# Performance work log

Measured on AMD Instinct MI355X. Metric: run time of the kernel, lower is better.

The kernel has to match this reference:

```python
import jax, jax.numpy as jnp
import numpy as np

N, R, A, F, T, O = 50000, 5, 8, 128, 2, 128
RADIUS = 1.0

def _template_vertices():
    # polar grid of template vertices in cartesian coords, shape (R, A, 2)
    radii = (np.arange(1, R + 1) / R) * RADIUS
    angles = np.linspace(0.0, 2.0 * np.pi, A, endpoint=False)
    x = radii[:, None] * np.cos(angles)[None, :]
    y = radii[:, None] * np.sin(angles)[None, :]
    return np.stack([x, y], axis=-1)

def _interp_coeffs():
    # Gaussian interpolation coefficients (concrete define_interpolation_coefficients),
    # shape (R, A, R*A), rows normalized -- constant, non-trainable (built in build()).
    v = _template_vertices().reshape(R * A, 2)
    d2 = ((v[:, None, :] - v[None, :, :]) ** 2).sum(-1)
    sigma = RADIUS / R
    w = np.exp(-d2 / (2.0 * sigma ** 2))
    w = w / w.sum(axis=1, keepdims=True)
    return w.reshape(R, A, R * A).astype(np.float32)

def setup_inputs() -> dict:
    key = jax.random.key(0)
    k1, k2, k3, k4, k5 = jax.random.split(key, 5)
    mesh_signal = jax.random.normal(k1, (N, F), dtype=jnp.float32)
    bary_w = jax.random.uniform(k2, (N, R, A, 3), dtype=jnp.float32)
    bary_w = bary_w / bary_w.sum(axis=-1, keepdims=True)  # barycentric weights sum to 1
    bary_idx = jax.random.randint(k3, (N, R, A, 3), 0, N, dtype=jnp.int32)
    glorot = lambda k, shp: jax.random.uniform(
        k, shp, jnp.float32, -1.0, 1.0) * np.sqrt(6.0 / (shp[-1] + shp[-2]))
    template_weights = glorot(k4, (A, T, O, F))  # (n_angular, templates, out, feat)
    bias = glorot(k5, (T, O))
    return {"mesh_signal": mesh_signal, "bary_w": bary_w,
            "template_weights": template_weights, "bias": bias,
            "interp_coeffs": jnp.asarray(_interp_coeffs()),
            "bary_idx": bary_idx}

def reference(mesh_signal, bary_w, template_weights, bias, interp_coeffs, bary_idx):
    # --- patch operator: barycentric gather + interpolation ---
    gathered = mesh_signal[bary_idx]                       # (N,R,A,3,F) irregular gather
    interp = (bary_w[..., None] * gathered).sum(axis=-2)   # (N,R,A,F)
    # prior: mix all R*A template-vertex signals per output template vertex
    sig = interp.reshape(-1, R * A, F)                     # (N,RA,F)
    interp = jnp.einsum('nkf,rak->nraf', sig, interp_coeffs)  # (N,R,A,F)
    # --- fold: all A rotations (rotation_delta=1), vectorized by rolling weights ---
    rots = jnp.arange(0, A, 1)                             # K = A rotations
    idx = (jnp.arange(A)[None, :] + rots[:, None]) % A     # (K,A): roll(interp,+r) == roll(W,-r)
    W_all = template_weights[idx]                          # (K,A,T,O,F)
    # TF adds bias before summing over (R,A) axes -> bias appears R*A times
    z = jnp.einsum('nraf,katof->nkto', interp, W_all) + (R * A) * bias  # (N,K,T,O)
    out = jax.nn.relu(z).sum(axis=2)                       # sum over templates -> (N,K,O)
    return out
```

## Files before the change

kernel.cpp:

```cpp
#include <hip/hip_runtime.h>
#include <hip/hip_bf16.h>
#include <stdint.h>

#define NN 50000
#define RR 5
#define AA 8
#define FF 128
#define TT 2
#define OO 128
#define KDIM 1024
#define KB 512
#define RA 40

typedef __attribute__((ext_vector_type(8))) short short8;
typedef __attribute__((ext_vector_type(4))) float f32x4;
typedef __attribute__((ext_vector_type(2))) float f32x2;
typedef __attribute__((ext_vector_type(4))) int i32x4;
typedef __attribute__((ext_vector_type(2))) unsigned u32x2;

#if __has_builtin(__builtin_elementwise_fma)
__device__ inline f32x2 pk_fma(f32x2 a, f32x2 b, f32x2 c) {
  return __builtin_elementwise_fma(a, b, c);
}
#else
__device__ inline f32x2 pk_fma(f32x2 a, f32x2 b, f32x2 c) {
  f32x2 d;
  asm("v_pk_fma_f32 %0, %1, %2, %3" : "=v"(d) : "v"(a), "v"(b), "v"(c));
  return d;
}
#endif

__device__ inline void gload_lds16(const void* g, void* l) {
  __builtin_amdgcn_global_load_lds(
      (const __attribute__((address_space(1))) unsigned int*)g,
      (__attribute__((address_space(3))) unsigned int*)l, 16, 0, 0);
}

__global__ void prep_kernel(const float* __restrict__ mesh,
                            const float* __restrict__ coeffs,
                            const float* __restrict__ W,
                            const float* __restrict__ bary_w,
                            const int* __restrict__ bary_idx,
                            __hip_bfloat16* __restrict__ meshq,
                            float* __restrict__ G,
                            __hip_bfloat16* __restrict__ B2,
                            unsigned* __restrict__ packb,
                            int do_pack) {
  int tid = blockIdx.x * blockDim.x + threadIdx.x;
  int stride = gridDim.x * blockDim.x;
  for (int i = tid; i < NN * FF; i += stride) {
    int n = i >> 7, f = i & 127;
    int p = f >> 5, fo = f & 31;
    meshq[((long)p * NN + n) * 32 + fo] = __float2bfloat16(mesh[i]);
  }
  for (int i = tid; i < AA * RA; i += stride) {
    int p = i / RA, k = i % RA;
    int a = p & 3;
    float s1 = 0.f, s2 = 0.f;
    for (int r = 0; r < RR; ++r) {
      s1 += coeffs[(r * AA + a) * RA + k];
      s2 += coeffs[(r * AA + a + 4) * RA + k];
    }
    G[i] = (p < 4) ? (s1 + s2) : (s1 - s2);
  }
  for (int e = tid; e < 2048 * KB; e += stride) {
    int sub = e & 7;
    int lane = (e >> 3) & 63;
    int kt = (e >> 9) & 15;
    int cg = (e >> 13) & 63;
    int half = e >> 19;
    int c = cg * 16 + (lane & 15);
    int k = kt * 32 + (lane >> 4) * 8 + sub;
    int o = c >> 3, t = (c >> 2) & 1, j = c & 3;
    int a4 = k >> 7, f = k & 127;
    int m = (a4 + j) & 3;
    float w0 = W[((m * TT + t) * OO + o) * FF + f];
    float w4 = W[(((m + 4) * TT + t) * OO + o) * FF + f];
    float v;
    if (half == 0) v = 0.5f * (w0 + w4);
    else {
      v = 0.5f * (w0 - w4);
      if (a4 + j >= 4) v = -v;
    }
    B2[e] = __float2bfloat16(v);
  }
  if (do_pack) {
    for (int i = tid; i < NN * 120; i += stride) {
      __hip_bfloat16 h = __float2bfloat16(bary_w[i]);
      unsigned wb = *(unsigned short*)&h;
      packb[i] = ((unsigned)bary_idx[i] << 16) | wb;
    }
  }
}

__global__ __launch_bounds__(256) void s_pass_packed(
    const __hip_bfloat16* __restrict__ meshq,
    const unsigned* __restrict__ packb,
    const float* __restrict__ G,
    __hip_bfloat16* __restrict__ Sout,
    int p) {
  __shared__ unsigned pk_s[32 * 120];
  __shared__ float g_s[AA * RA];
  int tid = threadIdx.x;
  long n0 = (long)blockIdx.x * 32;
  int nnode = (NN - n0 < 32) ? (int)(NN - n0) : 32;
  int nvec = nnode * 30;
  const i32x4* psrc = (const i32x4*)(packb + n0 * 120);
  for (int i = tid; i < nvec; i += 256) {
    i32x4 v = __builtin_nontemporal_load(psrc + i);
    ((i32x4*)pk_s)[i] = v;
  }
  for (int i = tid; i < AA * RA; i += 256) g_s[i] = G[i];
  __syncthreads();

  int g = tid >> 3;
  int fo = tid & 7;
  long n = n0 + g;
  if (n >= NN) return;
  const unsigned* pg = pk_s + g * 120;
  const char* mbase = (const char*)meshq + (long)p * NN * 64 + fo * 8;

  f32x2 accA[AA], accB[AA];
#pragma unroll
  for (int a = 0; a < AA; ++a) {
    accA[a] = (f32x2){0.f, 0.f};
    accB[a] = (f32x2){0.f, 0.f};
  }

#pragma unroll 2
  for (int k = 0; k < RA; ++k) {
    f32x2 sA = (f32x2){0.f, 0.f}, sB = (f32x2){0.f, 0.f};
#pragma unroll
    for (int j = 0; j < 3; ++j) {
      unsigned v = pg[k * 3 + j];
      long row = v >> 16;
      float w = __uint_as_float(v << 16);
      f32x2 wv = (f32x2){w, w};
      u32x2 u = *(const u32x2*)(mbase + row * 64);
      f32x2 lo = (f32x2){__uint_as_float(u[0] << 16),
                         __uint_as_float(u[0] & 0xffff0000u)};
      f32x2 hi = (f32x2){__uint_as_float(u[1] << 16),
                         __uint_as_float(u[1] & 0xffff0000u)};
      sA = pk_fma(wv, lo, sA);
      sB = pk_fma(wv, hi, sB);
    }
#pragma unroll
    for (int a = 0; a < AA; ++a) {
      float cc = g_s[a * RA + k];
      f32x2 cv = (f32x2){cc, cc};
      accA[a] = pk_fma(cv, sA, accA[a]);
      accB[a] = pk_fma(cv, sB, accB[a]);
    }
  }

  long base = n * KDIM + p * 32 + fo * 4;
#pragma unroll
  for (int a = 0; a < AA; ++a) {
    __hip_bfloat16 h0 = __float2bfloat16(accA[a][0]);
    __hip_bfloat16 h1 = __float2bfloat16(accA[a][1]);
    __hip_bfloat16 h2 = __float2bfloat16(accB[a][0]);
    __hip_bfloat16 h3 = __float2bfloat16(accB[a][1]);
    unsigned w0 = (unsigned)*(unsigned short*)&h0 |
                  ((unsigned)*(unsigned short*)&h1 << 16);
    unsigned w1 = (unsigned)*(unsigned short*)&h2 |
                  ((unsigned)*(unsigned short*)&h3 << 16);
    u32x2 st = (u32x2){w0, w1};
    __builtin_nontemporal_store(st, (u32x2*)(Sout + base + a * FF));
  }
}

__global__ __launch_bounds__(256) void s_pass_kernel(
    const __hip_bfloat16* __restrict__ meshq,
    const float* __restrict__ bary_w,
    const int* __restrict__ bary_idx,
    const float* __restrict__ G,
    __hip_bfloat16* __restrict__ Sout,
    int p) {
  __shared__ float w_s[16 * 120];
  __shared__ int i_s[16 * 120];
  __shared__ float g_s[AA * RA];
  int tid = threadIdx.x;
  long n0 = (long)blockIdx.x * 16;
  const f32x4* wsrc = (const f32x4*)(bary_w + n0 * 120);
  const i32x4* isrc = (const i32x4*)(bary_idx + n0 * 120);
  for (int i = tid; i < 480; i += 256) {
    f32x4 wv = __builtin_nontemporal_load(wsrc + i);
    ((f32x4*)w_s)[i] = wv;
    i32x4 iv = __builtin_nontemporal_load(isrc + i);
    ((i32x4*)i_s)[i] = iv;
  }
  for (int i = tid; i < AA * RA; i += 256) g_s[i] = G[i];
  __syncthreads();
  int g = tid >> 4;
  int fo = tid & 15;
  long n = n0 + g;
  const float* wg = w_s + g * 120;
  const int* ig = i_s + g * 120;
  const char* mbase = (const char*)meshq + (long)p * NN * 64 + fo * 4;
  float sx_acc[AA], sy_acc[AA];
#pragma unroll
  for (int a = 0; a < AA; ++a) { sx_acc[a] = 0.f; sy_acc[a] = 0.f; }
#pragma unroll 2
  for (int k = 0; k < RA; ++k) {
    float sx = 0.f, sy = 0.f;
#pragma unroll
    for (int j = 0; j < 3; ++j) {
      int row = ig[k * 3 + j];
      unsigned u = *(const unsigned*)(mbase + (long)row * 64);
      float w = wg[k * 3 + j];
      sx += w * __uint_as_float(u << 16);
      sy += w * __uint_as_float(u & 0xffff0000u);
    }
#pragma unroll
    for (int a = 0; a < AA; ++a) {
      float c = g_s[a * RA + k];
      sx_acc[a] += c * sx;
      sy_acc[a] += c * sy;
    }
  }
  long base = n * KDIM + p * 32 + fo * 2;
#pragma unroll
  for (int a = 0; a < AA; ++a) {
    __hip_bfloat16 hx = __float2bfloat16(sx_acc[a]);
    __hip_bfloat16 hy = __float2bfloat16(sy_acc[a]);
    unsigned u = (unsigned)*(unsigned short*)&hx | ((unsigned)*(unsigned short*)&hy << 16);
    __builtin_nontemporal_store(u, (unsigned*)(Sout + base + a * FF));
  }
}

__global__ __launch_bounds__(256, 3) void gemm_kernel(
    const __hip_bfloat16* __restrict__ Sh,
    const __hip_bfloat16* __restrict__ B2,
    const float* __restrict__ bias,
    float* __restrict__ out) {
  int bx = blockIdx.x;
  int by = blockIdx.y;
  int cb = by & 7;
  int mt = ((by >> 3) << 3) + bx;
  if (mt >= 782) return;
  int row0 = mt * 64;

  int tid = threadIdx.x;
  int lane = tid & 63;
  int wid = tid >> 6;
  int wave_m = wid >> 1;
  int wave_n = wid & 1;

  __shared__ __align__(16) char lds[49152];

  long srcA[2];
  int dstA[2];
#pragma unroll
  for (int i = 0; i < 2; ++i) {
    int li = i * 256 + tid;
    int plane = li >> 8;
    int r = (li & 255) >> 2, sp = li & 3;
    int sl = sp ^ ((r >> 1) & 3);
    int rowA = row0 + r;
    if (rowA >= NN) rowA = NN - 1;
    srcA[i] = (long)rowA * KDIM + plane * 512 + sl * 8;
    dstA[i] = li * 16;
  }
  const char* b2c = (const char*)B2;
  long srcB[4];
  int dstB[4];
#pragma unroll
  for (int i = 0; i < 4; ++i) {
    int li = i * 256 + tid;
    int half = li >> 9, cgl = (li >> 6) & 7, inner = li & 63;
    srcB[i] = (((long)(half * 64 + cb * 8 + cgl) * 16) * 1024) + inner * 16;
    dstB[i] = 8192 + li * 16;
  }
  int offA[2];
#pragma unroll
  for (int m = 0; m < 2; ++m) {
    int r = wave_m * 32 + m * 16 + (lane & 15);
    int phys = (lane >> 4) ^ ((r >> 1) & 3);
    offA[m] = r * 64 + phys * 16;
  }
  int offB[4];
#pragma unroll
  for (int n = 0; n < 4; ++n)
    offB[n] = 8192 + (wave_n * 4 + n) * 1024 + lane * 16;

  f32x4 acc[2][8];
#pragma unroll
  for (int m = 0; m < 2; ++m)
#pragma unroll
    for (int q = 0; q < 8; ++q) acc[m][q] = (f32x4){0.f, 0.f, 0.f, 0.f};

#define STAGE(T)                                                              \
  {                                                                           \
    char* base_ = lds + ((T) & 1) * 24576;                                    \
    long k0_ = (long)(T) * 32;                                                \
    _Pragma("unroll") for (int i_ = 0; i_ < 2; ++i_)                          \
        gload_lds16(Sh + srcA[i_] + k0_, base_ + dstA[i_]);                   \
    _Pragma("unroll") for (int i_ = 0; i_ < 4; ++i_)                          \
        gload_lds16(b2c + srcB[i_] + (long)(T) * 1024, base_ + dstB[i_]);     \
  }

#define GSTEP(STP, DOSTAGE)                                                   \
  {                                                                           \
    const char* cbuf = lds + ((STP) & 1) * 24576;                             \
    asm volatile("s_waitcnt vmcnt(0)" ::: "memory");                          \
    __builtin_amdgcn_sched_barrier(0);                                        \
    __builtin_amdgcn_s_barrier();                                             \
    __builtin_amdgcn_sched_barrier(0);                                        \
    if (DOSTAGE) STAGE((STP) + 1)                                             \
    __builtin_amdgcn_sched_barrier(0);                                        \
    short8 aE[2], aO[2], bE[4], bO[4];                                        \
    _Pragma("unroll") for (int m_ = 0; m_ < 2; ++m_) {                        \
      aE[m_] = *(const short8*)(cbuf + offA[m_]);                             \
      aO[m_] = *(const short8*)(cbuf + offA[m_] + 4096);                      \
    }                                                                         \
    _Pragma("unroll") for (int n_ = 0; n_ < 4; ++n_) {                        \
      bE[n_] = *(const short8*)(cbuf + offB[n_]);                             \
      bO[n_] = *(const short8*)(cbuf + offB[n_] + 8192);                      \
    }                                                                         \
    __builtin_amdgcn_s_setprio(1);                                            \
    _Pragma("unroll") for (int m_ = 0; m_ < 2; ++m_)                          \
        _Pragma("unroll") for (int n_ = 0; n_ < 4; ++n_) {                    \
      acc[m_][n_] = __builtin_amdgcn_mfma_f32_16x16x32_bf16(                  \
          aE[m_], bE[n_], acc[m_][n_], 0, 0, 0);                              \
      acc[m_][n_ + 4] = __builtin_amdgcn_mfma_f32_16x16x32_bf16(              \
          aO[m_], bO[n_], acc[m_][n_ + 4], 0, 0, 0);                          \
    }                                                                         \
    __builtin_amdgcn_s_setprio(0);                                            \
    __builtin_amdgcn_sched_barrier(0);                                        \
  }

  STAGE(0)
  GSTEP(0, 1)  GSTEP(1, 1)  GSTEP(2, 1)  GSTEP(3, 1)
  GSTEP(4, 1)  GSTEP(5, 1)  GSTEP(6, 1)  GSTEP(7, 1)
  GSTEP(8, 1)  GSTEP(9, 1)  GSTEP(10, 1) GSTEP(11, 1)
  GSTEP(12, 1) GSTEP(13, 1) GSTEP(14, 1) GSTEP(15, 0)

  __syncthreads();
  float* lout = (float*)lds;
  int c = lane & 15;
  int t = (c >> 2) & 1;
  int j = c & 3;
  int hi = lane >> 4;
  float bq[4];
#pragma unroll
  for (int n = 0; n < 4; ++n) {
    int o_l = wave_n * 8 + n * 2 + (c >> 3);
    bq[n] = 40.f * bias[t * OO + cb * 16 + o_l];
  }
#pragma unroll
  for (int m = 0; m < 2; ++m) {
#pragma unroll
    for (int n = 0; n < 4; ++n) {
      int o_l = wave_n * 8 + n * 2 + (c >> 3);
#pragma unroll
      for (int i = 0; i < 4; ++i) {
        float zE = acc[m][n][i];
        float zO = acc[m][n + 4][i];
        float rlo = fmaxf(zE + zO + bq[n], 0.f);
        float rhi = fmaxf(zE - zO + bq[n], 0.f);
        rlo += __shfl_xor(rlo, 4);
        rhi += __shfl_xor(rhi, 4);
        if (!(lane & 4)) {
          int cl = wave_m * 32 + m * 16 + hi * 4 + i;
          lout[cl * 156 + j * 20 + o_l] = rlo;
          lout[cl * 156 + (j + 4) * 20 + o_l] = rhi;
        }
      }
    }
  }
  __syncthreads();
#pragma unroll
  for (int it = 0; it < 8; ++it) {
    int gi = it * 256 + tid;
    int cl = gi >> 5;
    int rem = gi & 31;
    int kr = rem >> 2, q = rem & 3;
    int grow = row0 + cl;
    if (grow < NN) {
      f32x4 v = *(const f32x4*)(lout + cl * 156 + kr * 20 + q * 4);
      long gaddr = (long)grow * 1024 + kr * 128 + cb * 16 + q * 4;
      __builtin_nontemporal_store(v, (f32x4*)(out + gaddr));
    }
  }
}

extern "C" void kernel_launch(void* const* d_in, const int* in_sizes, int n_in,
                              void* d_out, int out_size, void* d_ws, size_t ws_size,
                              hipStream_t stream) {
  const float* mesh   = (const float*)d_in[0];
  const float* bary_w = (const float*)d_in[1];
  const float* W      = (const float*)d_in[2];
  const float* bias   = (const float*)d_in[3];
  const float* coeffs = (const float*)d_in[4];
  const int* bidx     = (const int*)d_in[5];
  float* out = (float*)d_out;
  char* ws = (char*)d_ws;

  __hip_bfloat16* meshq = (__hip_bfloat16*)ws;
  float* G              = (float*)(ws + 12800000);
  __hip_bfloat16* B2    = (__hip_bfloat16*)(ws + 12801280);
  __hip_bfloat16* Smat  = (__hip_bfloat16*)(ws + 16995584);
  unsigned* packb       = (unsigned*)(ws + 119395584);

  int do_pack = (ws_size >= 143395584UL) ? 1 : 0;

  prep_kernel<<<dim3(2048), dim3(256), 0, stream>>>(mesh, coeffs, W, bary_w, bidx,
                                                    meshq, G, B2, packb, do_pack);
  if (do_pack) {
    for (int p = 0; p < 4; ++p)
      s_pass_packed<<<dim3(1563), dim3(256), 0, stream>>>(meshq, packb, G, Smat, p);
  } else {
    for (int p = 0; p < 4; ++p)
      s_pass_kernel<<<dim3(3125), dim3(256), 0, stream>>>(meshq, bary_w, bidx, G, Smat, p);
  }
  gemm_kernel<<<dim3(8, 784), dim3(256), 0, stream>>>(Smat, B2, bias, out);
}
```

Baseline: 374.1 us.

## Split GEMM waves by K-half instead of M to reuse A fragments

Reassigns the four waves so each pair handles one half (even/odd plane) of the K data across all 64 rows, rather than splitting rows. Each wave now loads 4 A and 4 B fragments per step instead of 4 A and 8 B, which cuts LDS read traffic per MFMA. The partial accumulators of the two halves must then be combined through LDS in the epilogue, done in four row slices with extra barriers and a narrower, serialized output store phase.

```diff
diff --git a/kernel.cpp b/kernel.cpp
--- a/kernel.cpp
+++ b/kernel.cpp
@@ -243,8 +243,8 @@
   int tid = threadIdx.x;
   int lane = tid & 63;
   int wid = tid >> 6;
-  int wave_m = wid >> 1;
-  int wave_n = wid & 1;
+  int half = wid >> 1;
+  int wn = wid & 1;
 
   __shared__ __align__(16) char lds[49152];
 
@@ -267,27 +267,27 @@
 #pragma unroll
   for (int i = 0; i < 4; ++i) {
     int li = i * 256 + tid;
-    int half = li >> 9, cgl = (li >> 6) & 7, inner = li & 63;
-    srcB[i] = (((long)(half * 64 + cb * 8 + cgl) * 16) * 1024) + inner * 16;
+    int hf = li >> 9, cgl = (li >> 6) & 7, inner = li & 63;
+    srcB[i] = (((long)(hf * 64 + cb * 8 + cgl) * 16) * 1024) + inner * 16;
     dstB[i] = 8192 + li * 16;
   }
-  int offA[2];
-#pragma unroll
-  for (int m = 0; m < 2; ++m) {
-    int r = wave_m * 32 + m * 16 + (lane & 15);
+  int offA[4];
+#pragma unroll
+  for (int m = 0; m < 4; ++m) {
+    int r = m * 16 + (lane & 15);
     int phys = (lane >> 4) ^ ((r >> 1) & 3);
-    offA[m] = r * 64 + phys * 16;
+    offA[m] = half * 4096 + r * 64 + phys * 16;
   }
   int offB[4];
 #pragma unroll
   for (int n = 0; n < 4; ++n)
-    offB[n] = 8192 + (wave_n * 4 + n) * 1024 + lane * 16;
-
-  f32x4 acc[2][8];
-#pragma unroll
-  for (int m = 0; m < 2; ++m)
-#pragma unroll
-    for (int q = 0; q < 8; ++q) acc[m][q] = (f32x4){0.f, 0.f, 0.f, 0.f};
+    offB[n] = 8192 + half * 8192 + (wn * 4 + n) * 1024 + lane * 16;
+
+  f32x4 acc[4][4];
+#pragma unroll
+  for (int m = 0; m < 4; ++m)
+#pragma unroll
+    for (int n = 0; n < 4; ++n) acc[m][n] = (f32x4){0.f, 0.f, 0.f, 0.f};
 
 #define STAGE(T)                                                              \
   {                                                                           \
@@ -308,23 +308,16 @@
     __builtin_amdgcn_sched_barrier(0);                                        \
     if (DOSTAGE) STAGE((STP) + 1)                                             \
     __builtin_amdgcn_sched_barrier(0);                                        \
-    short8 aE[2], aO[2], bE[4], bO[4];                                        \
-    _Pragma("unroll") for (int m_ = 0; m_ < 2; ++m_) {                        \
-      aE[m_] = *(const short8*)(cbuf + offA[m_]);                             \
-      aO[m_] = *(const short8*)(cbuf + offA[m_] + 4096);                      \
-    }                                                                         \
-    _Pragma("unroll") for (int n_ = 0; n_ < 4; ++n_) {                        \
-      bE[n_] = *(const short8*)(cbuf + offB[n_]);                             \
-      bO[n_] = *(const short8*)(cbuf + offB[n_] + 8192);                      \
-    }                                                                         \
+    short8 aF[4], bF[4];                                                      \
+    _Pragma("unroll") for (int m_ = 0; m_ < 4; ++m_)                          \
+        aF[m_] = *(const short8*)(cbuf + offA[m_]);                           \
+    _Pragma("unroll") for (int n_ = 0; n_ < 4; ++n_)                          \
+        bF[n_] = *(const short8*)(cbuf + offB[n_]);                           \
     __builtin_amdgcn_s_setprio(1);                                            \
-    _Pragma("unroll") for (int m_ = 0; m_ < 2; ++m_)                          \
-        _Pragma("unroll") for (int n_ = 0; n_ < 4; ++n_) {                    \
-      acc[m_][n_] = __builtin_amdgcn_mfma_f32_16x16x32_bf16(                  \
-          aE[m_], bE[n_], acc[m_][n_], 0, 0, 0);                              \
-      acc[m_][n_ + 4] = __builtin_amdgcn_mfma_f32_16x16x32_bf16(              \
-          aO[m_], bO[n_], acc[m_][n_ + 4], 0, 0, 0);                          \
-    }                                                                         \
+    _Pragma("unroll") for (int m_ = 0; m_ < 4; ++m_)                          \
+        _Pragma("unroll") for (int n_ = 0; n_ < 4; ++n_)                      \
+            acc[m_][n_] = __builtin_amdgcn_mfma_f32_16x16x32_bf16(            \
+                aF[m_], bF[n_], acc[m_][n_], 0, 0, 0);                        \
     __builtin_amdgcn_s_setprio(0);                                            \
     __builtin_amdgcn_sched_barrier(0);                                        \
   }
@@ -335,51 +328,52 @@
   GSTEP(8, 1)  GSTEP(9, 1)  GSTEP(10, 1) GSTEP(11, 1)
   GSTEP(12, 1) GSTEP(13, 1) GSTEP(14, 1) GSTEP(15, 0)
 
-  __syncthreads();
-  float* lout = (float*)lds;
-  int c = lane & 15;
-  int t = (c >> 2) & 1;
-  int j = c & 3;
-  int hi = lane >> 4;
-  float bq[4];
-#pragma unroll
-  for (int n = 0; n < 4; ++n) {
-    int o_l = wave_n * 8 + n * 2 + (c >> 3);
-    bq[n] = 40.f * bias[t * OO + cb * 16 + o_l];
-  }
-#pragma unroll
-  for (int m = 0; m < 2; ++m) {
-#pragma unroll
-    for (int n = 0; n < 4; ++n) {
-      int o_l = wave_n * 8 + n * 2 + (c >> 3);
-#pragma unroll
-      for (int i = 0; i < 4; ++i) {
-        float zE = acc[m][n][i];
-        float zO = acc[m][n + 4][i];
-        float rlo = fmaxf(zE + zO + bq[n], 0.f);
-        float rhi = fmaxf(zE - zO + bq[n], 0.f);
-        rlo += __shfl_xor(rlo, 4);
-        rhi += __shfl_xor(rhi, 4);
-        if (!(lane & 4)) {
-          int cl = wave_m * 32 + m * 16 + hi * 4 + i;
-          lout[cl * 156 + j * 20 + o_l] = rlo;
-          lout[cl * 156 + (j + 4) * 20 + o_l] = rhi;
+  float* estg = (float*)lds;
+  float* lout = (float*)(lds + 8192);
+#pragma unroll
+  for (int m = 0; m < 4; ++m) {
+    __syncthreads();
+    if (half == 0) {
+#pragma unroll
+      for (int n = 0; n < 4; ++n)
+        *(f32x4*)(estg + ((wn * 4 + n) * 64 + lane) * 4) = acc[m][n];
+    }
+    __syncthreads();
+    if (half == 1) {
+#pragma unroll
+      for (int n = 0; n < 4; ++n) {
+        f32x4 e = *(const f32x4*)(estg + ((wn * 4 + n) * 64 + lane) * 4);
+        int cc = wn * 64 + n * 16 + (lane & 15);
+        int o_l = cc >> 3;
+        int j = cc & 3;
+        float bqv = 40.f * bias[((cc >> 2) & 1) * OO + cb * 16 + o_l];
+#pragma unroll
+        for (int i = 0; i < 4; ++i) {
+          float rlo = fmaxf(e[i] + acc[m][n][i] + bqv, 0.f);
+          float rhi = fmaxf(e[i] - acc[m][n][i] + bqv, 0.f);
+          rlo += __shfl_xor(rlo, 4);
+          rhi += __shfl_xor(rhi, 4);
+          if (!(lane & 4)) {
+            int cl = (lane >> 4) * 4 + i;
+            lout[cl * 156 + j * 20 + o_l] = rlo;
+            lout[cl * 156 + (j + 4) * 20 + o_l] = rhi;
+          }
         }
       }
     }
-  }
-  __syncthreads();
-#pragma unroll
-  for (int it = 0; it < 8; ++it) {
-    int gi = it * 256 + tid;
-    int cl = gi >> 5;
-    int rem = gi & 31;
-    int kr = rem >> 2, q = rem & 3;
-    int grow = row0 + cl;
-    if (grow < NN) {
-      f32x4 v = *(const f32x4*)(lout + cl * 156 + kr * 20 + q * 4);
-      long gaddr = (long)grow * 1024 + kr * 128 + cb * 16 + q * 4;
-      __builtin_nontemporal_store(v, (f32x4*)(out + gaddr));
+    __syncthreads();
+#pragma unroll
+    for (int it = 0; it < 2; ++it) {
+      int gi = it * 256 + tid;
+      int cl = gi >> 5;
+      int rem = gi & 31;
+      int kr = rem >> 2, q = rem & 3;
+      int grow = row0 + m * 16 + cl;
+      if (grow < NN) {
+        f32x4 v = *(const f32x4*)(lout + cl * 156 + kr * 20 + q * 4);
+        long gaddr = (long)grow * 1024 + kr * 128 + cb * 16 + q * 4;
+        __builtin_nontemporal_store(v, (f32x4*)(out + gaddr));
+      }
     }
   }
 }
```

Result: slower. 409.3 us (+9.4%).
